# Performance work log

Measured on AMD Instinct MI355X. Metric: run time of the kernel, lower is better.

The kernel has to match this reference:

```python
import jax, jax.numpy as jnp
import numpy as np

TEMP = 0.05            # self.temp
NUM_INSTANCES = 16     # self.num_instances


def _l2norm(x):
    return x / jnp.linalg.norm(x, axis=-1, keepdims=True)


def setup_inputs() -> dict:
    key = jax.random.key(0)
    ks = jax.random.split(key, 6)
    B, D, N, K, NDATA = 256, 2048, 32768, 8192, 100000
    inputs = jax.random.normal(ks[0], (B, D), jnp.float32)
    # memory bank rows are kept unit-norm by the momentum update; init normalized
    features = _l2norm(jax.random.normal(ks[1], (N, D), jnp.float32))
    kmeans_centeroids = jax.random.normal(ks[2], (K, D), jnp.float32)
    targets = jax.random.randint(ks[3], (B,), 0, N)
    kmeans_pids = jax.random.randint(ks[4], (NDATA,), 0, K)
    indexes = jax.random.randint(ks[5], (B,), 0, NDATA)
    return {"inputs": inputs, "features": features,
            "kmeans_centeroids": kmeans_centeroids, "targets": targets,
            "kmeans_pids": kmeans_pids, "indexes": indexes, "neg_size": 20}


def reference(inputs, features, kmeans_centeroids, targets, kmeans_pids,
              indexes, neg_size):
    B = inputs.shape[0]
    K = kmeans_centeroids.shape[0]
    x = _l2norm(inputs)                                   # F.normalize(inputs, dim=1)
    outputs = x @ features.T                              # CM.forward: [B, N]
    finch_pos = jnp.take_along_axis(outputs, targets[:, None], axis=1)  # [B,1]
    kmeans_score = x @ kmeans_centeroids.T                # [B, K]
    batch_kmeans_pids = kmeans_pids[indexes]              # [B]
    # scatter_(-2) own kmeans cluster, then take top-neg_size negatives
    masked = jax.lax.stop_gradient(kmeans_score)          # detach().clone()
    masked = masked.at[jnp.arange(B), batch_kmeans_pids].set(-2.0)
    _, sel_ind_neg = jax.lax.top_k(masked, neg_size)      # [B, neg_size]
    kmeans_chosen_neg = jnp.take_along_axis(kmeans_score, sel_ind_neg, axis=1)
    mixed_score = jnp.concatenate([finch_pos, kmeans_chosen_neg], axis=1) / TEMP
    # confidence mask: per group of NUM_INSTANCES (first half of batch),
    # sample agrees with the group's modal kmeans pid (np.bincount().argmax())
    half = B // 2
    g = batch_kmeans_pids[:half].reshape(-1, NUM_INSTANCES)        # [G, I]
    counts = jax.nn.one_hot(g, K, dtype=jnp.int32).sum(axis=1)     # [G, K]
    mode = jnp.argmax(counts, axis=1)                              # ties -> smallest id
    mask_half = (g == mode[:, None]).reshape(-1).astype(jnp.float32)
    confidence_mask = jnp.concatenate([mask_half, mask_half])      # [B]
    # CE(mixed_score, 0) per-sample, confidence-weighted mean
    ce_neg = -jax.nn.log_softmax(mixed_score, axis=1)[:, 0]
    neg_con_loss = (confidence_mask * ce_neg).mean()
    # CE(outputs/temp, targets) mean
    logp = jax.nn.log_softmax(outputs / TEMP, axis=1)
    ce_main = -jnp.take_along_axis(logp, targets[:, None], axis=1).mean()
    return 0.2 * neg_con_loss + ce_main
```

## Files before the change

### kernel.cpp

```cpp
#include <hip/hip_runtime.h>
#include <stdint.h>

typedef __attribute__((ext_vector_type(8))) short short8;
typedef __attribute__((ext_vector_type(4))) float floatx4;

__device__ __forceinline__ unsigned short f2b(float f) {
    union { float f; uint32_t u; } v; v.f = f;
    uint32_t u = v.u;
    return (unsigned short)((u + 0x7FFFu + ((u >> 16) & 1u)) >> 16);
}

__device__ __forceinline__ void async16(const void* g, void* l) {
    __builtin_amdgcn_global_load_lds(
        (const __attribute__((address_space(1))) void*)g,
        (__attribute__((address_space(3))) void*)l, 16, 0, 0);
}

__global__ void norm_kernel(const float* __restrict__ in,
                            unsigned short* __restrict__ xb, int D) {
    int b = blockIdx.x, t = threadIdx.x;
    const float* row = in + (size_t)b * D;
    float ss = 0.f;
    for (int i = t * 4; i < D; i += 1024) {
        float4 v = *(const float4*)(row + i);
        ss += v.x * v.x + v.y * v.y + v.z * v.z + v.w * v.w;
    }
    for (int off = 32; off > 0; off >>= 1) ss += __shfl_down(ss, off);
    __shared__ float wsum[4];
    __shared__ float rn_sh;
    if ((t & 63) == 0) wsum[t >> 6] = ss;
    __syncthreads();
    if (t == 0) rn_sh = rsqrtf(wsum[0] + wsum[1] + wsum[2] + wsum[3]);
    __syncthreads();
    float rn = rn_sh;
    unsigned short* orow = xb + (size_t)b * D;
    for (int i = t * 4; i < D; i += 1024) {
        float4 v = *(const float4*)(row + i);
        ushort4 o;
        o.x = f2b(v.x * rn); o.y = f2b(v.y * rn);
        o.z = f2b(v.z * rn); o.w = f2b(v.w * rn);
        *(ushort4*)(orow + i) = o;
    }
}

__global__ __launch_bounds__(256, 2)
void gemm_kernel(const unsigned short* __restrict__ xb,
                 const float* __restrict__ featB,
                 const float* __restrict__ centB,
                 const int* __restrict__ targets,
                 float* __restrict__ S, float* __restrict__ pos,
                 float* __restrict__ km,
                 int D, int N, int K, int nbF) {
    __shared__ __align__(16) unsigned short Alds[256 * 32];
    __shared__ __align__(16) unsigned short Blds[64 * 32];

    const int t = threadIdx.x;
    const int w = t >> 6, l = t & 63;
    const bool isFeat = ((int)blockIdx.x < nbF);
    const int n0 = (isFeat ? (int)blockIdx.x : ((int)blockIdx.x - nbF)) * 64;
    const float* Bsrc = isFeat ? featB : centB;

    floatx4 acc[4][4];
#pragma unroll
    for (int ti = 0; ti < 4; ++ti)
#pragma unroll
        for (int tj = 0; tj < 4; ++tj)
            acc[ti][tj] = (floatx4){0.f, 0.f, 0.f, 0.f};

    const int kIters = D / 32;
    const int br = t >> 2, bp = t & 3;
    const float* bptr = Bsrc + (size_t)(n0 + br) * D + bp * 8;

    for (int kt = 0; kt < kIters; ++kt) {
#pragma unroll
        for (int j = 0; j < 4; ++j) {
            int bo = (j * 256 + t) * 16;
            int arow = bo >> 6, ic = bo & 63;
            async16((const char*)xb + (size_t)arow * (D * 2) + (size_t)kt * 64 + ic,
                    (char*)Alds + bo);
        }
        {
            const float* bg = bptr + kt * 32;
            float4 f0 = *(const float4*)bg;
            float4 f1 = *(const float4*)(bg + 4);
            short8 bv;
            bv[0] = (short)f2b(f0.x); bv[1] = (short)f2b(f0.y);
            bv[2] = (short)f2b(f0.z); bv[3] = (short)f2b(f0.w);
            bv[4] = (short)f2b(f1.x); bv[5] = (short)f2b(f1.y);
            bv[6] = (short)f2b(f1.z); bv[7] = (short)f2b(f1.w);
            *(short8*)((char*)Blds + br * 64 + bp * 16) = bv;
        }
        __syncthreads();

        short8 aF[4], bF[4];
#pragma unroll
        for (int ti = 0; ti < 4; ++ti)
            aF[ti] = *(const short8*)((const char*)Alds +
                      (w * 64 + ti * 16 + (l & 15)) * 64 + ((l >> 4) * 16));
#pragma unroll
        for (int tj = 0; tj < 4; ++tj)
            bF[tj] = *(const short8*)((const char*)Blds +
                      (tj * 16 + (l & 15)) * 64 + ((l >> 4) * 16));
#pragma unroll
        for (int ti = 0; ti < 4; ++ti)
#pragma unroll
            for (int tj = 0; tj < 4; ++tj)
                acc[ti][tj] = __builtin_amdgcn_mfma_f32_16x16x32_bf16(
                    aF[ti], bF[tj], acc[ti][tj], 0, 0, 0);
        __syncthreads();
    }

    if (isFeat) {
#pragma unroll
        for (int ti = 0; ti < 4; ++ti) {
#pragma unroll
            for (int r = 0; r < 4; ++r) {
                int row = w * 64 + ti * 16 + ((l >> 4) << 2) + r;
                int tr = targets[row];
                int col0 = n0 + (l & 15);
                float e = 0.f;
#pragma unroll
                for (int tj = 0; tj < 4; ++tj) {
                    float c = acc[ti][tj][r];
                    e += __expf(c * 20.0f);
                    if (tr == col0 + tj * 16) pos[row] = c;
                }
                e += __shfl_xor(e, 1); e += __shfl_xor(e, 2);
                e += __shfl_xor(e, 4); e += __shfl_xor(e, 8);
                if ((l & 15) == 0) atomicAdd(&S[row], e);
            }
        }
    } else {
#pragma unroll
        for (int ti = 0; ti < 4; ++ti) {
#pragma unroll
            for (int r = 0; r < 4; ++r) {
                int row = w * 64 + ti * 16 + ((l >> 4) << 2) + r;
                size_t base = (size_t)row * K + n0 + (l & 15);
#pragma unroll
                for (int tj = 0; tj < 4; ++tj)
                    km[base + tj * 16] = acc[ti][tj][r];
            }
        }
    }
}

__global__ void topk_kernel(const float* __restrict__ km,
                            const int* __restrict__ pids,
                            const int* __restrict__ idxs,
                            const int* __restrict__ negsz,
                            float* __restrict__ topv, int K) {
    __shared__ float sv[8192];
    __shared__ float rv[256];
    __shared__ int ri[256];
    int b = blockIdx.x, t = threadIdx.x;
    const float* row = km + (size_t)b * K;
    for (int i = t; i < K; i += 256) sv[i] = row[i];
    __syncthreads();
    if (t == 0) sv[pids[idxs[b]]] = -1e30f;
    int ns = *negsz; if (ns > 32) ns = 32;
    __syncthreads();
    for (int j = 0; j < ns; ++j) {
        float best = -1e30f; int bi = 0;
        for (int i = t; i < K; i += 256) {
            float v = sv[i];
            if (v > best) { best = v; bi = i; }
        }
        rv[t] = best; ri[t] = bi;
        __syncthreads();
        for (int s = 128; s > 0; s >>= 1) {
            if (t < s && rv[t + s] > rv[t]) { rv[t] = rv[t + s]; ri[t] = ri[t + s]; }
            __syncthreads();
        }
        if (t == 0) { topv[b * 32 + j] = rv[0]; sv[ri[0]] = -1e30f; }
        __syncthreads();
    }
}

__global__ void final_kernel(const float* __restrict__ S,
                             const float* __restrict__ pos,
                             const float* __restrict__ topv,
                             const int* __restrict__ pids,
                             const int* __restrict__ idxs,
                             const int* __restrict__ negsz,
                             float* __restrict__ out, int B) {
    __shared__ int pid_sh[256];
    __shared__ int mode_sh[16];
    __shared__ float red[256];
    int t = threadIdx.x;
    if (t < B) pid_sh[t] = pids[idxs[t]];
    __syncthreads();
    int half = B >> 1;
    int G = half / 16;
    if (t < G) {
        int bestPid = 0x7FFFFFFF, bestCnt = -1;
        for (int i = 0; i < 16; ++i) {
            int p = pid_sh[t * 16 + i];
            int c = 0;
            for (int j = 0; j < 16; ++j) c += (pid_sh[t * 16 + j] == p) ? 1 : 0;
            if (c > bestCnt || (c == bestCnt && p < bestPid)) { bestCnt = c; bestPid = p; }
        }
        mode_sh[t] = bestPid;
    }
    __syncthreads();
    float contrib = 0.f;
    if (t < B) {
        int hb = (t < half) ? t : t - half;
        float mask = (pid_sh[hb] == mode_sh[hb / 16]) ? 1.f : 0.f;
        int ns = *negsz; if (ns > 32) ns = 32;
        float p20 = pos[t] * 20.0f;
        float m = p20;
        for (int j = 0; j < ns; ++j) m = fmaxf(m, topv[t * 32 + j] * 20.0f);
        float se = __expf(p20 - m);
        for (int j = 0; j < ns; ++j) se += __expf(topv[t * 32 + j] * 20.0f - m);
        float ce_neg = m + logf(se) - p20;
        float ce_main = logf(S[t]) - p20;
        contrib = (0.2f * mask * ce_neg + ce_main) / (float)B;
    }
    red[t] = contrib;
    __syncthreads();
    for (int s = 128; s > 0; s >>= 1) {
        if (t < s) red[t] += red[t + s];
        __syncthreads();
    }
    if (t == 0) out[0] = red[0];
}

extern "C" void kernel_launch(void* const* d_in, const int* in_sizes, int n_in,
                              void* d_out, int out_size, void* d_ws, size_t ws_size,
                              hipStream_t stream) {
    const float* inputs   = (const float*)d_in[0];
    const float* features = (const float*)d_in[1];
    const float* cents    = (const float*)d_in[2];
    const int*   targets  = (const int*)d_in[3];
    const int*   pids     = (const int*)d_in[4];
    const int*   idxs     = (const int*)d_in[5];
    const int*   negsz    = (const int*)d_in[6];
    float* out = (float*)d_out;

    int Bb = in_sizes[3];
    int Dd = in_sizes[0] / Bb;
    int Nn = in_sizes[1] / Dd;
    int Kk = in_sizes[2] / Dd;

    char* ws = (char*)d_ws;
    unsigned short* xb = (unsigned short*)ws;
    size_t o = (size_t)Bb * Dd * 2;
    float* km   = (float*)(ws + o); o += (size_t)Bb * Kk * 4;
    float* S    = (float*)(ws + o); o += (size_t)Bb * 4;
    float* pos  = (float*)(ws + o); o += (size_t)Bb * 4;
    float* topv = (float*)(ws + o); o += (size_t)Bb * 32 * 4;

    hipMemsetAsync(S, 0, (size_t)Bb * 4, stream);
    norm_kernel<<<Bb, 256, 0, stream>>>(inputs, xb, Dd);
    int nbF = Nn / 64, nbC = Kk / 64;
    gemm_kernel<<<nbF + nbC, 256, 0, stream>>>(xb, features, cents, targets,
                                               S, pos, km, Dd, Nn, Kk, nbF);
    topk_kernel<<<Bb, 256, 0, stream>>>(km, pids, idxs, negsz, topv, Kk);
    final_kernel<<<1, 256, 0, stream>>>(S, pos, topv, pids, idxs, negsz, out, Bb);
}
```

Measured before the change: 554.3 us.

## Double GEMM K-tile with XOR-swizzled LDS and register-resident top-k

The GEMM K-tile grows from 32 to 64, halving the number of barrier pairs per block. Both LDS tiles use an XOR swizzle to reduce bank conflicts on fragment reads. The B conversion uses a cheaper packed bf16 round that drops the ties-to-even correction. Top-k now keeps each row in registers (32 values per thread) and reduces with wave shuffles instead of a shared-memory tree, cutting barriers per selection, but it assumes K equals 8192.

```diff
diff --git a/kernel.cpp b/kernel.cpp
--- a/kernel.cpp
+++ b/kernel.cpp
@@ -8,6 +8,12 @@
     union { float f; uint32_t u; } v; v.f = f;
     uint32_t u = v.u;
     return (unsigned short)((u + 0x7FFFu + ((u >> 16) & 1u)) >> 16);
+}
+
+__device__ __forceinline__ uint32_t pk2(float a, float b) {
+    union { float f; uint32_t u; } x, y; x.f = a; y.f = b;
+    uint32_t ua = x.u + 0x8000u, ub = y.u + 0x8000u;
+    return (ua >> 16) | (ub & 0xFFFF0000u);
 }
 
 __device__ __forceinline__ void async16(const void* g, void* l) {
@@ -43,6 +49,7 @@
     }
 }
 
+#define BKk 64
 __global__ __launch_bounds__(256, 2)
 void gemm_kernel(const unsigned short* __restrict__ xb,
                  const float* __restrict__ featB,
@@ -50,9 +57,9 @@
                  const int* __restrict__ targets,
                  float* __restrict__ S, float* __restrict__ pos,
                  float* __restrict__ km,
-                 int D, int N, int K, int nbF) {
-    __shared__ __align__(16) unsigned short Alds[256 * 32];
-    __shared__ __align__(16) unsigned short Blds[64 * 32];
+                 int D, int K, int nbF) {
+    __shared__ __align__(16) unsigned short Alds[256 * BKk];
+    __shared__ __align__(16) unsigned short Blds[64 * BKk];
 
     const int t = threadIdx.x;
     const int w = t >> 6, l = t & 63;
@@ -67,46 +74,63 @@
         for (int tj = 0; tj < 4; ++tj)
             acc[ti][tj] = (floatx4){0.f, 0.f, 0.f, 0.f};
 
-    const int kIters = D / 32;
-    const int br = t >> 2, bp = t & 3;
-    const float* bptr = Bsrc + (size_t)(n0 + br) * D + bp * 8;
+    const int kIters = D / BKk;
+    const int brow = t >> 2, bq = t & 3;
+    const float* bg0 = Bsrc + (size_t)(n0 + brow) * D + bq * 16;
+    const int bc0 = ((bq * 2) ^ (brow & 7)) * 16;
+    const int bc1 = ((bq * 2 + 1) ^ (brow & 7)) * 16;
+    const char* xbB = (const char*)xb;
 
     for (int kt = 0; kt < kIters; ++kt) {
 #pragma unroll
-        for (int j = 0; j < 4; ++j) {
-            int bo = (j * 256 + t) * 16;
-            int arow = bo >> 6, ic = bo & 63;
-            async16((const char*)xb + (size_t)arow * (D * 2) + (size_t)kt * 64 + ic,
-                    (char*)Alds + bo);
+        for (int j = 0; j < 8; ++j) {
+            int slin = j * 256 + t;
+            int r = slin >> 3;
+            int cg = (slin & 7) ^ (r & 7);
+            async16(xbB + (size_t)r * (D * 2) + kt * (BKk * 2) + cg * 16,
+                    (char*)Alds + slin * 16);
         }
         {
-            const float* bg = bptr + kt * 32;
-            float4 f0 = *(const float4*)bg;
+            const float* bg = bg0 + kt * BKk;
+            float4 f0 = *(const float4*)(bg);
             float4 f1 = *(const float4*)(bg + 4);
-            short8 bv;
-            bv[0] = (short)f2b(f0.x); bv[1] = (short)f2b(f0.y);
-            bv[2] = (short)f2b(f0.z); bv[3] = (short)f2b(f0.w);
-            bv[4] = (short)f2b(f1.x); bv[5] = (short)f2b(f1.y);
-            bv[6] = (short)f2b(f1.z); bv[7] = (short)f2b(f1.w);
-            *(short8*)((char*)Blds + br * 64 + bp * 16) = bv;
-        }
-        __syncthreads();
-
-        short8 aF[4], bF[4];
-#pragma unroll
-        for (int ti = 0; ti < 4; ++ti)
-            aF[ti] = *(const short8*)((const char*)Alds +
-                      (w * 64 + ti * 16 + (l & 15)) * 64 + ((l >> 4) * 16));
-#pragma unroll
-        for (int tj = 0; tj < 4; ++tj)
-            bF[tj] = *(const short8*)((const char*)Blds +
-                      (tj * 16 + (l & 15)) * 64 + ((l >> 4) * 16));
-#pragma unroll
-        for (int ti = 0; ti < 4; ++ti)
-#pragma unroll
-            for (int tj = 0; tj < 4; ++tj)
-                acc[ti][tj] = __builtin_amdgcn_mfma_f32_16x16x32_bf16(
-                    aF[ti], bF[tj], acc[ti][tj], 0, 0, 0);
+            float4 f2 = *(const float4*)(bg + 8);
+            float4 f3 = *(const float4*)(bg + 12);
+            uint4 p0, p1;
+            p0.x = pk2(f0.x, f0.y); p0.y = pk2(f0.z, f0.w);
+            p0.z = pk2(f1.x, f1.y); p0.w = pk2(f1.z, f1.w);
+            p1.x = pk2(f2.x, f2.y); p1.y = pk2(f2.z, f2.w);
+            p1.z = pk2(f3.x, f3.y); p1.w = pk2(f3.z, f3.w);
+            char* bb = (char*)Blds + brow * 128;
+            *(uint4*)(bb + bc0) = p0;
+            *(uint4*)(bb + bc1) = p1;
+        }
+        __syncthreads();
+
+#pragma unroll
+        for (int s = 0; s < 2; ++s) {
+            short8 aF[4], bF[4];
+#pragma unroll
+            for (int ti = 0; ti < 4; ++ti) {
+                int R = w * 64 + ti * 16 + (l & 15);
+                int g = s * 4 + (l >> 4);
+                aF[ti] = *(const short8*)((const char*)Alds +
+                          R * 128 + ((g ^ (R & 7)) * 16));
+            }
+#pragma unroll
+            for (int tj = 0; tj < 4; ++tj) {
+                int Rn = tj * 16 + (l & 15);
+                int g = s * 4 + (l >> 4);
+                bF[tj] = *(const short8*)((const char*)Blds +
+                          Rn * 128 + ((g ^ (Rn & 7)) * 16));
+            }
+#pragma unroll
+            for (int ti = 0; ti < 4; ++ti)
+#pragma unroll
+                for (int tj = 0; tj < 4; ++tj)
+                    acc[ti][tj] = __builtin_amdgcn_mfma_f32_16x16x32_bf16(
+                        aF[ti], bF[tj], acc[ti][tj], 0, 0, 0);
+        }
         __syncthreads();
     }
 
@@ -145,34 +169,54 @@
     }
 }
 
-__global__ void topk_kernel(const float* __restrict__ km,
-                            const int* __restrict__ pids,
-                            const int* __restrict__ idxs,
-                            const int* __restrict__ negsz,
-                            float* __restrict__ topv, int K) {
-    __shared__ float sv[8192];
-    __shared__ float rv[256];
-    __shared__ int ri[256];
+__global__ __launch_bounds__(256, 4)
+void topk_kernel(const float* __restrict__ kmr,
+                 const int* __restrict__ pids,
+                 const int* __restrict__ idxs,
+                 const int* __restrict__ negsz,
+                 float* __restrict__ topv, int K) {
     int b = blockIdx.x, t = threadIdx.x;
-    const float* row = km + (size_t)b * K;
-    for (int i = t; i < K; i += 256) sv[i] = row[i];
-    __syncthreads();
-    if (t == 0) sv[pids[idxs[b]]] = -1e30f;
+    int w = t >> 6, l = t & 63;
+    const float* row = kmr + (size_t)b * K;
+    float v[32];
+#pragma unroll
+    for (int k = 0; k < 32; ++k) v[k] = row[k * 256 + t];
+    int gi = pids[idxs[b]];
+    if ((gi & 255) == t) {
+        int kk = gi >> 8;
+#pragma unroll
+        for (int k = 0; k < 32; ++k) if (k == kk) v[k] = -1e30f;
+    }
+    float bv = v[0]; int bk = 0;
+#pragma unroll
+    for (int k = 1; k < 32; ++k) if (v[k] > bv) { bv = v[k]; bk = k; }
+
+    __shared__ float rv[4];
+    __shared__ int rg[4];
     int ns = *negsz; if (ns > 32) ns = 32;
-    __syncthreads();
     for (int j = 0; j < ns; ++j) {
-        float best = -1e30f; int bi = 0;
-        for (int i = t; i < K; i += 256) {
-            float v = sv[i];
-            if (v > best) { best = v; bi = i; }
-        }
-        rv[t] = best; ri[t] = bi;
-        __syncthreads();
-        for (int s = 128; s > 0; s >>= 1) {
-            if (t < s && rv[t + s] > rv[t]) { rv[t] = rv[t + s]; ri[t] = ri[t + s]; }
-            __syncthreads();
-        }
-        if (t == 0) { topv[b * 32 + j] = rv[0]; sv[ri[0]] = -1e30f; }
+        float mv = bv; int mg = bk * 256 + t;
+#pragma unroll
+        for (int off = 1; off < 64; off <<= 1) {
+            float ov = __shfl_xor(mv, off);
+            int og = __shfl_xor(mg, off);
+            if (ov > mv) { mv = ov; mg = og; }
+        }
+        if (l == 0) { rv[w] = mv; rg[w] = mg; }
+        __syncthreads();
+        float gv = rv[0]; int gg = rg[0];
+#pragma unroll
+        for (int ww = 1; ww < 4; ++ww)
+            if (rv[ww] > gv) { gv = rv[ww]; gg = rg[ww]; }
+        if (t == 0) topv[b * 32 + j] = gv;
+        if ((gg & 255) == t) {
+            int kk = gg >> 8;
+#pragma unroll
+            for (int k = 0; k < 32; ++k) if (k == kk) v[k] = -1e30f;
+            bv = v[0]; bk = 0;
+#pragma unroll
+            for (int k = 1; k < 32; ++k) if (v[k] > bv) { bv = v[k]; bk = k; }
+        }
         __syncthreads();
     }
 }
@@ -255,7 +299,7 @@
     norm_kernel<<<Bb, 256, 0, stream>>>(inputs, xb, Dd);
     int nbF = Nn / 64, nbC = Kk / 64;
     gemm_kernel<<<nbF + nbC, 256, 0, stream>>>(xb, features, cents, targets,
-                                               S, pos, km, Dd, Nn, Kk, nbF);
+                                               S, pos, km, Dd, Kk, nbF);
     topk_kernel<<<Bb, 256, 0, stream>>>(km, pids, idxs, negsz, topv, Kk);
     final_kernel<<<1, 256, 0, stream>>>(S, pos, topv, pids, idxs, negsz, out, Bb);
 }
```

New measurement: 493.9 us. 10.9% less time.
